# Kernel optimization log

Measured on AMD Instinct MI355X. Metric: run time of the kernel, lower is better.

## Reference

```python
import jax, jax.numpy as jnp
import numpy as np

T, B, C = 2048, 4, 512
H, K, P = 16, 31, 15  # num_heads, kernel_size, padding_l
R = C // H


def setup_inputs() -> dict:
    key = jax.random.key(0)
    ks = jax.random.split(key, 6)
    x = jax.random.normal(ks[0], (T, B, C), dtype=jnp.float32)
    s = 0.02
    W1 = jax.random.normal(ks[1], (C, C), dtype=jnp.float32) * s   # linear1 weight
    b1 = jnp.zeros((C,), dtype=jnp.float32)
    Wl = jax.random.normal(ks[2], (H * K, C), dtype=jnp.float32) * s  # weight_linear (no bias)
    W2 = jax.random.normal(ks[3], (C, C), dtype=jnp.float32) * s   # linear2 weight
    b2 = jnp.zeros((C,), dtype=jnp.float32)
    return {"x": x, "W1": W1, "b1": b1, "Wl": Wl, "W2": W2, "b2": b2}


def _dynamic_conv(h, Wl):
    # h: (T, B, C). Generate per-position per-head filters, softmax over K,
    # then banded weighted sum over a local window of K timesteps.
    w = jnp.einsum('tbc,kc->tbk', h, Wl).reshape(T, B, H, K)
    w = jax.nn.softmax(w, axis=-1)                      # weight_softmax=True
    # pad left P, right K-1-P ("same" window: position t sees h[t-P : t-P+K])
    hp = jnp.pad(h, ((P, K - 1 - P), (0, 0), (0, 0)))   # (T+K-1, B, C)
    idx = jnp.arange(T)[:, None] + jnp.arange(K)[None, :]  # (T, K)
    hw = hp[idx].reshape(T, K, B, H, R)                 # unfolded windows
    return jnp.einsum('tkbhr,tbhk->tbhr', hw, w).reshape(T, B, C)


def reference(x, W1, b1, Wl, W2, b2):
    h = jnp.einsum('tbc,dc->tbd', x, W1) + b1           # linear1 (glu=False -> no act)
    out = _dynamic_conv(h, Wl)                          # conv_bias=False
    out = jnp.einsum('tbc,dc->tbd', out, W2) + b2       # linear2
    return out
```

## Files before the change

kernel.cpp:

```cpp
#include <hip/hip_runtime.h>
#include <hip/hip_bf16.h>

#define TT 2048
#define BB 4
#define CC 512
#define HH 16
#define KK 31
#define PP 15
#define MM (TT*BB)
#define NPAD 512

typedef __bf16 bf16x8 __attribute__((ext_vector_type(8)));
typedef float f32x4 __attribute__((ext_vector_type(4)));
typedef unsigned short ushort8 __attribute__((ext_vector_type(8)));
typedef unsigned short ushort4v __attribute__((ext_vector_type(4)));

__device__ __forceinline__ float bf2f(unsigned short u) {
    return __uint_as_float(((unsigned int)u) << 16);
}
__device__ __forceinline__ unsigned short f2bf(float f) {
    unsigned int x = __float_as_uint(f);
    x += 0x7fffu + ((x >> 16) & 1u);
    return (unsigned short)(x >> 16);
}

__global__ __launch_bounds__(256) void cast_all(const float* __restrict__ x,
                                                const float* __restrict__ W1,
                                                const float* __restrict__ Wl,
                                                const float* __restrict__ W2,
                                                unsigned short* __restrict__ xb,
                                                unsigned short* __restrict__ W1b,
                                                unsigned short* __restrict__ Wlb,
                                                unsigned short* __restrict__ W2b) {
    const int b = blockIdx.x;
    if (b < 4096) {
        const int i = b * 1024 + threadIdx.x * 4;
        const float4 v = *(const float4*)&x[i];
        ushort4v o = { f2bf(v.x), f2bf(v.y), f2bf(v.z), f2bf(v.w) };
        *(ushort4v*)&xb[i] = o;
        return;
    }
    const int bb = b - 4096;
    const int i = (bb & 255) * 1024 + threadIdx.x * 4;
    const float* src;
    unsigned short* dst;
    int n_src = 262144;
    if (bb < 256)      { src = W1; dst = W1b; }
    else if (bb < 512) { src = Wl; dst = Wlb; n_src = HH * KK * CC; }
    else               { src = W2; dst = W2b; }
    ushort4v o = {0, 0, 0, 0};
    if (i < n_src) {
        const float4 v = *(const float4*)&src[i];
        o[0] = f2bf(v.x); o[1] = f2bf(v.y); o[2] = f2bf(v.z); o[3] = f2bf(v.w);
    }
    *(ushort4v*)&dst[i] = o;
}

#define GBM 128
#define GBN 64
#define GBK 64
#define KC  512
#define NT  8

#define STAGE(kt, buf)                                                                             \
    do {                                                                                           \
        const int k0_ = (kt) * GBK;                                                                \
        _Pragma("unroll")                                                                          \
        for (int j = 0; j < 2; ++j)                                                                \
            __builtin_amdgcn_global_load_lds(                                                      \
                (const __attribute__((address_space(1))) void*)(gA[j] + k0_),                      \
                (__attribute__((address_space(3))) void*)(&As[buf][0] + (j * 512 + wv * 64) * 8),  \
                16, 0, 0);                                                                         \
        __builtin_amdgcn_global_load_lds(                                                          \
            (const __attribute__((address_space(1))) void*)(gB0 + k0_),                            \
            (__attribute__((address_space(3))) void*)(&Bs[buf][0] + wv * 64 * 8),                  \
            16, 0, 0);                                                                             \
    } while (0)

template<bool OUT_BF16>
__global__ __launch_bounds__(512, 4) void gemm_nt_mfma(const unsigned short* __restrict__ A,
                                                       const unsigned short* __restrict__ B,
                                                       const float* __restrict__ bias,
                                                       void* __restrict__ Cout,
                                                       int N, int nn) {
    __shared__ short As[3][GBM * GBK];
    __shared__ short Bs[3][GBN * GBK];

    const int tid = threadIdx.x;
    const int l   = tid & 63;
    const int wv  = tid >> 6;
    const int wr  = wv >> 1;
    const int wc  = wv & 1;

    const int s  = (blockIdx.x & 7) * (gridDim.x >> 3) + (blockIdx.x >> 3);
    const int bm = (s / nn) * GBM;
    const int bn = (s % nn) * GBN;

    const unsigned short* gA[2];
    #pragma unroll
    for (int j = 0; j < 2; ++j) {
        const int slot = j * 512 + tid;
        const int r  = slot >> 3;
        const int sl = (slot & 7) ^ (r & 7);
        gA[j] = A + (size_t)(bm + r) * KC + sl * 8;
    }
    const int rB  = tid >> 3;
    const int slB = (tid & 7) ^ (rB & 7);
    const unsigned short* gB0 = B + (size_t)(bn + rB) * KC + slB * 8;

    f32x4 acc[2][2] = {};

    const int lr = l & 15;
    const int ls = l >> 4;
    int offA[2][2], offB[2][2];
    #pragma unroll
    for (int mi = 0; mi < 2; ++mi) {
        const int r = wr * 32 + mi * 16 + lr;
        #pragma unroll
        for (int ks = 0; ks < 2; ++ks)
            offA[mi][ks] = r * 64 + (((ks * 4 + ls) ^ (r & 7)) * 8);
    }
    #pragma unroll
    for (int ni = 0; ni < 2; ++ni) {
        const int r = wc * 32 + ni * 16 + lr;
        #pragma unroll
        for (int ks = 0; ks < 2; ++ks)
            offB[ni][ks] = r * 64 + (((ks * 4 + ls) ^ (r & 7)) * 8);
    }

    STAGE(0, 0);
    STAGE(1, 1);

    #pragma unroll
    for (int kt = 0; kt < NT; ++kt) {
        if (kt < NT - 1) asm volatile("s_waitcnt vmcnt(3)" ::: "memory");
        else             asm volatile("s_waitcnt vmcnt(0)" ::: "memory");
        __builtin_amdgcn_s_barrier();
        if (kt + 2 < NT) STAGE(kt + 2, (kt + 2) % 3);

        const int cb = kt % 3;
        bf16x8 af[2][2], bfv[2][2];
        #pragma unroll
        for (int mi = 0; mi < 2; ++mi)
            #pragma unroll
            for (int ks = 0; ks < 2; ++ks)
                af[mi][ks] = *(const bf16x8*)&As[cb][offA[mi][ks]];
        #pragma unroll
        for (int ni = 0; ni < 2; ++ni)
            #pragma unroll
            for (int ks = 0; ks < 2; ++ks)
                bfv[ni][ks] = *(const bf16x8*)&Bs[cb][offB[ni][ks]];

        #pragma unroll
        for (int mi = 0; mi < 2; ++mi)
            #pragma unroll
            for (int ni = 0; ni < 2; ++ni)
                #pragma unroll
                for (int ks = 0; ks < 2; ++ks)
                    acc[mi][ni] = __builtin_amdgcn_mfma_f32_16x16x32_bf16(af[mi][ks], bfv[ni][ks], acc[mi][ni], 0, 0, 0);
    }

    #pragma unroll
    for (int mi = 0; mi < 2; ++mi) {
        const int row0 = bm + wr * 32 + mi * 16 + ls * 4;
        #pragma unroll
        for (int ni = 0; ni < 2; ++ni) {
            const int col = bn + wc * 32 + ni * 16 + lr;
            const float bv = bias ? bias[col] : 0.0f;
            #pragma unroll
            for (int j = 0; j < 4; ++j) {
                const float v = acc[mi][ni][j] + bv;
                if (OUT_BF16)
                    ((unsigned short*)Cout)[(size_t)(row0 + j) * N + col] = f2bf(v);
                else
                    ((float*)Cout)[(size_t)(row0 + j) * N + col] = v;
            }
        }
    }
}

__global__ __launch_bounds__(64) void dynconv_fused(const unsigned short* __restrict__ hb,
                                                    const unsigned short* __restrict__ lgb,
                                                    unsigned short* __restrict__ cvb) {
    __shared__ float w_s[64][33];

    const int bid = blockIdx.x;
    const int u   = (bid & 7) * 256 + (bid >> 3);
    const int tg  = u >> 2;
    const int b   = u & 3;
    const int t0  = tg * 4;
    const int tid = threadIdx.x;

    {
        const int dt = tid >> 4, hd = tid & 15;
        const unsigned short* lp = lgb + (size_t)((t0 + dt) * BB + b) * NPAD + hd * KK;
        float e[32];
        #pragma unroll
        for (int v8 = 0; v8 < 4; ++v8) {
            const ushort8 lv = *(const ushort8*)&lp[v8 * 8];
            #pragma unroll
            for (int j = 0; j < 8; ++j) e[v8 * 8 + j] = bf2f(lv[j]);
        }
        float mx = -1e30f;
        #pragma unroll
        for (int k = 0; k < KK; ++k) mx = fmaxf(mx, e[k]);
        float sm = 0.f;
        #pragma unroll
        for (int k = 0; k < KK; ++k) { e[k] = __expf(e[k] - mx); sm += e[k]; }
        const float inv = 1.f / sm;
        #pragma unroll
        for (int k = 0; k < KK; ++k) w_s[tid][k] = e[k] * inv;
    }
    __syncthreads();

    const int c0 = tid * 8;
    const int hd = tid >> 2;
    float acc[4][8] = {};
    #pragma unroll
    for (int j = 0; j < 34; ++j) {
        const int tt = t0 - PP + j;
        if ((unsigned)tt >= TT) continue;
        const ushort8 hv = *(const ushort8*)&hb[(size_t)((tt * BB + b) * CC) + c0];
        float hf[8];
        #pragma unroll
        for (int cc = 0; cc < 8; ++cc) hf[cc] = bf2f(hv[cc]);
        #pragma unroll
        for (int dt = 0; dt < 4; ++dt) {
            const int k = j - dt;
            if ((unsigned)k >= KK) continue;
            const float wk = w_s[dt * 16 + hd][k];
            #pragma unroll
            for (int cc = 0; cc < 8; ++cc) acc[dt][cc] = fmaf(hf[cc], wk, acc[dt][cc]);
        }
    }
    #pragma unroll
    for (int dt = 0; dt < 4; ++dt) {
        ushort8 o;
        #pragma unroll
        for (int cc = 0; cc < 8; ++cc) o[cc] = f2bf(acc[dt][cc]);
        *(ushort8*)&cvb[(size_t)(((t0 + dt) * BB + b) * CC) + c0] = o;
    }
}

extern "C" void kernel_launch(void* const* d_in, const int* in_sizes, int n_in,
                              void* d_out, int out_size, void* d_ws, size_t ws_size,
                              hipStream_t stream) {
    const float* x  = (const float*)d_in[0];
    const float* W1 = (const float*)d_in[1];
    const float* b1 = (const float*)d_in[2];
    const float* Wl = (const float*)d_in[3];
    const float* W2 = (const float*)d_in[4];
    const float* b2 = (const float*)d_in[5];
    float* out = (float*)d_out;

    unsigned short* xb  = (unsigned short*)d_ws;
    unsigned short* hb  = xb  + (size_t)MM * CC;
    unsigned short* cvb = hb  + (size_t)MM * CC;
    unsigned short* W1b = cvb + (size_t)MM * CC;
    unsigned short* Wlb = W1b + (size_t)CC * CC;
    unsigned short* W2b = Wlb + (size_t)NPAD * CC;
    unsigned short* lgb = W2b + (size_t)CC * CC;

    cast_all<<<4096 + 768, 256, 0, stream>>>(x, W1, Wl, W2, xb, W1b, Wlb, W2b);

    const int nblk = (MM / GBM) * (CC / GBN);

    gemm_nt_mfma<true><<<nblk, 512, 0, stream>>>(xb, W1b, b1, hb, CC, CC / GBN);
    gemm_nt_mfma<true><<<nblk, 512, 0, stream>>>(hb, Wlb, nullptr, lgb, NPAD, NPAD / GBN);
    dynconv_fused<<<TT * BB / 4, 64, 0, stream>>>(hb, lgb, cvb);
    gemm_nt_mfma<false><<<nblk, 512, 0, stream>>>(cvb, W2b, b2, out, CC, CC / GBN);
}
```

Baseline: 50.50 us.

## Use 1024-thread GEMM blocks with one 16-row MFMA tile per wave

Doubles the GEMM block to 16 waves so that each wave computes a 16x32 output slice instead of 32x32. The tile loads are respread: every wave loads part of A, and waves 8-15 also load B. The wait counts are adjusted per wave group to match. The aim is more waves in flight to hide LDS and global latency. In exchange, each wave reuses its fragments less, LDS reads per MFMA go up, and barrier cost grows with larger blocks.

```diff
diff --git a/kernel.cpp b/kernel.cpp
--- a/kernel.cpp
+++ b/kernel.cpp
@@ -65,24 +65,23 @@
 #define STAGE(kt, buf)                                                                             \
     do {                                                                                           \
         const int k0_ = (kt) * GBK;                                                                \
-        _Pragma("unroll")                                                                          \
-        for (int j = 0; j < 2; ++j)                                                                \
+        __builtin_amdgcn_global_load_lds(                                                          \
+            (const __attribute__((address_space(1))) void*)(gA0 + k0_),                            \
+            (__attribute__((address_space(3))) void*)(&As[buf][0] + wv * 512),                     \
+            16, 0, 0);                                                                             \
+        if (wv >= 8)                                                                               \
             __builtin_amdgcn_global_load_lds(                                                      \
-                (const __attribute__((address_space(1))) void*)(gA[j] + k0_),                      \
-                (__attribute__((address_space(3))) void*)(&As[buf][0] + (j * 512 + wv * 64) * 8),  \
+                (const __attribute__((address_space(1))) void*)(gB0 + k0_),                        \
+                (__attribute__((address_space(3))) void*)(&Bs[buf][0] + (wv - 8) * 512),           \
                 16, 0, 0);                                                                         \
-        __builtin_amdgcn_global_load_lds(                                                          \
-            (const __attribute__((address_space(1))) void*)(gB0 + k0_),                            \
-            (__attribute__((address_space(3))) void*)(&Bs[buf][0] + wv * 64 * 8),                  \
-            16, 0, 0);                                                                             \
     } while (0)
 
 template<bool OUT_BF16>
-__global__ __launch_bounds__(512, 4) void gemm_nt_mfma(const unsigned short* __restrict__ A,
-                                                       const unsigned short* __restrict__ B,
-                                                       const float* __restrict__ bias,
-                                                       void* __restrict__ Cout,
-                                                       int N, int nn) {
+__global__ __launch_bounds__(1024, 8) void gemm_nt_mfma(const unsigned short* __restrict__ A,
+                                                        const unsigned short* __restrict__ B,
+                                                        const float* __restrict__ bias,
+                                                        void* __restrict__ Cout,
+                                                        int N, int nn) {
     __shared__ short As[3][GBM * GBK];
     __shared__ short Bs[3][GBN * GBK];
 
@@ -96,29 +95,24 @@
     const int bm = (s / nn) * GBM;
     const int bn = (s % nn) * GBN;
 
-    const unsigned short* gA[2];
-    #pragma unroll
-    for (int j = 0; j < 2; ++j) {
-        const int slot = j * 512 + tid;
-        const int r  = slot >> 3;
-        const int sl = (slot & 7) ^ (r & 7);
-        gA[j] = A + (size_t)(bm + r) * KC + sl * 8;
-    }
-    const int rB  = tid >> 3;
-    const int slB = (tid & 7) ^ (rB & 7);
+    const int rA  = tid >> 3;
+    const int slA = (tid & 7) ^ (rA & 7);
+    const unsigned short* gA0 = A + (size_t)(bm + rA) * KC + slA * 8;
+    const int tB  = tid - 512;
+    const int rB  = (tB & 511) >> 3;
+    const int slB = (tB & 7) ^ (rB & 7);
     const unsigned short* gB0 = B + (size_t)(bn + rB) * KC + slB * 8;
 
-    f32x4 acc[2][2] = {};
+    f32x4 acc[2] = {};
 
     const int lr = l & 15;
     const int ls = l >> 4;
-    int offA[2][2], offB[2][2];
-    #pragma unroll
-    for (int mi = 0; mi < 2; ++mi) {
-        const int r = wr * 32 + mi * 16 + lr;
+    int offA[2], offB[2][2];
+    {
+        const int r = wr * 16 + lr;
         #pragma unroll
         for (int ks = 0; ks < 2; ++ks)
-            offA[mi][ks] = r * 64 + (((ks * 4 + ls) ^ (r & 7)) * 8);
+            offA[ks] = r * 64 + (((ks * 4 + ls) ^ (r & 7)) * 8);
     }
     #pragma unroll
     for (int ni = 0; ni < 2; ++ni) {
@@ -133,18 +127,20 @@
 
     #pragma unroll
     for (int kt = 0; kt < NT; ++kt) {
-        if (kt < NT - 1) asm volatile("s_waitcnt vmcnt(3)" ::: "memory");
-        else             asm volatile("s_waitcnt vmcnt(0)" ::: "memory");
+        if (kt < NT - 1) {
+            if (wv < 8) asm volatile("s_waitcnt vmcnt(1)" ::: "memory");
+            else        asm volatile("s_waitcnt vmcnt(2)" ::: "memory");
+        } else {
+            asm volatile("s_waitcnt vmcnt(0)" ::: "memory");
+        }
         __builtin_amdgcn_s_barrier();
         if (kt + 2 < NT) STAGE(kt + 2, (kt + 2) % 3);
 
         const int cb = kt % 3;
-        bf16x8 af[2][2], bfv[2][2];
-        #pragma unroll
-        for (int mi = 0; mi < 2; ++mi)
-            #pragma unroll
-            for (int ks = 0; ks < 2; ++ks)
-                af[mi][ks] = *(const bf16x8*)&As[cb][offA[mi][ks]];
+        bf16x8 af[2], bfv[2][2];
+        #pragma unroll
+        for (int ks = 0; ks < 2; ++ks)
+            af[ks] = *(const bf16x8*)&As[cb][offA[ks]];
         #pragma unroll
         for (int ni = 0; ni < 2; ++ni)
             #pragma unroll
@@ -152,24 +148,21 @@
                 bfv[ni][ks] = *(const bf16x8*)&Bs[cb][offB[ni][ks]];
 
         #pragma unroll
-        for (int mi = 0; mi < 2; ++mi)
-            #pragma unroll
-            for (int ni = 0; ni < 2; ++ni)
-                #pragma unroll
-                for (int ks = 0; ks < 2; ++ks)
-                    acc[mi][ni] = __builtin_amdgcn_mfma_f32_16x16x32_bf16(af[mi][ks], bfv[ni][ks], acc[mi][ni], 0, 0, 0);
-    }
-
-    #pragma unroll
-    for (int mi = 0; mi < 2; ++mi) {
-        const int row0 = bm + wr * 32 + mi * 16 + ls * 4;
+        for (int ni = 0; ni < 2; ++ni)
+            #pragma unroll
+            for (int ks = 0; ks < 2; ++ks)
+                acc[ni] = __builtin_amdgcn_mfma_f32_16x16x32_bf16(af[ks], bfv[ni][ks], acc[ni], 0, 0, 0);
+    }
+
+    {
+        const int row0 = bm + wr * 16 + ls * 4;
         #pragma unroll
         for (int ni = 0; ni < 2; ++ni) {
             const int col = bn + wc * 32 + ni * 16 + lr;
             const float bv = bias ? bias[col] : 0.0f;
             #pragma unroll
             for (int j = 0; j < 4; ++j) {
-                const float v = acc[mi][ni][j] + bv;
+                const float v = acc[ni][j] + bv;
                 if (OUT_BF16)
                     ((unsigned short*)Cout)[(size_t)(row0 + j) * N + col] = f2bf(v);
                 else
@@ -265,8 +258,8 @@
 
     const int nblk = (MM / GBM) * (CC / GBN);
 
-    gemm_nt_mfma<true><<<nblk, 512, 0, stream>>>(xb, W1b, b1, hb, CC, CC / GBN);
-    gemm_nt_mfma<true><<<nblk, 512, 0, stream>>>(hb, Wlb, nullptr, lgb, NPAD, NPAD / GBN);
+    gemm_nt_mfma<true><<<nblk, 1024, 0, stream>>>(xb, W1b, b1, hb, CC, CC / GBN);
+    gemm_nt_mfma<true><<<nblk, 1024, 0, stream>>>(hb, Wlb, nullptr, lgb, NPAD, NPAD / GBN);
     dynconv_fused<<<TT * BB / 4, 64, 0, stream>>>(hb, lgb, cvb);
-    gemm_nt_mfma<false><<<nblk, 512, 0, stream>>>(cvb, W2b, b2, out, CC, CC / GBN);
-}
+    gemm_nt_mfma<false><<<nblk, 1024, 0, stream>>>(cvb, W2b, b2, out, CC, CC / GBN);
+}
```

New measurement: 50.99 us. Within noise of the previous version (+1.0%).
